# Optimization experiments

Hardware: AMD Instinct MI355X
Metric: run time of the kernel (lower is better)

## Reference

```python
import jax, jax.numpy as jnp
import numpy as np

B, T, D, H, C = 8, 1024, 1024, 16, 8  # batch, seq, d_model, heads, num_concepts
DK = D // H
LAMBD = 5.0


def setup_inputs() -> dict:
    key = jax.random.key(0)
    ks = jax.random.split(key, 14)
    s = 0.02
    return {
        "qa_concept": jax.random.normal(ks[0], (B, T, T, C), jnp.float32),
        "query": jax.random.normal(ks[1], (B, T, D), jnp.float32),
        "key": jax.random.normal(ks[2], (B, T, D), jnp.float32),
        "value": jax.random.normal(ks[3], (B, T, D), jnp.float32),
        "Wq": jax.random.normal(ks[4], (D, D), jnp.float32) * s,
        "bq": jnp.zeros((D,), jnp.float32),
        "Wk": jax.random.normal(ks[5], (D, D), jnp.float32) * s,
        "bk": jnp.zeros((D,), jnp.float32),
        "Wv": jax.random.normal(ks[6], (D, D), jnp.float32) * s,
        "bv": jnp.zeros((D,), jnp.float32),
        "Wo": jax.random.normal(ks[7], (D, D), jnp.float32) * s,
        "bo": jnp.zeros((D,), jnp.float32),
        "mask": jax.random.randint(ks[8], (B, T), 0, 2, jnp.int32),
    }


def reference(qa_concept, query, key, value, Wq, bq, Wk, bk, Wv, bv, Wo, bo, mask):
    # Linear projections (torch Linear: y = x @ W.T + b)
    q = (query @ Wq.T + bq).reshape(B, T, H, DK).transpose(0, 2, 1, 3)  # [B,H,T,dk]
    k = (key @ Wk.T + bk).reshape(B, T, H, DK).transpose(0, 2, 1, 3)
    v = (value @ Wv.T + bv).reshape(B, T, H, DK).transpose(0, 2, 1, 3)
    scores = jnp.einsum("bhqd,bhkd->bhqk", q, k) / jnp.sqrt(jnp.float32(DK))
    # concept bias added to first C heads only
    bias = LAMBD * jnp.transpose(qa_concept, (0, 3, 1, 2))  # [B,C,T,T]
    scores = scores.at[:, :C, :, :].add(bias)
    # mask: [B,T] -> [B,1,1,T], fill -1e9 where 0
    scores = jnp.where(mask[:, None, None, :] == 0, jnp.float32(-1e9), scores)
    attn = jax.nn.softmax(scores, axis=-1)  # dropout is identity in eval
    x = jnp.einsum("bhqk,bhkd->bhqd", attn, v)
    x = x.transpose(0, 2, 1, 3).reshape(B, T, D)
    return x @ Wo.T + bo
```

## Files before the change

kernel.cpp:

```cpp
#include <hip/hip_runtime.h>

#define B_  8
#define T_  1024
#define D_  1024
#define H_  16
#define DK_ 64
#define C_  8
#define N_  (B_*T_)

typedef __attribute__((ext_vector_type(8))) short bf16x8;
typedef __attribute__((ext_vector_type(4))) float f32x4;
typedef __attribute__((ext_vector_type(8))) unsigned short u16x8;
typedef __attribute__((ext_vector_type(4))) unsigned short u16x4;

__device__ __forceinline__ float bf2f(unsigned short u) {
  union { unsigned int i; float f; } x; x.i = ((unsigned int)u) << 16; return x.f;
}
__device__ __forceinline__ unsigned short f2bf(float f) {
  union { float f; unsigned int i; } x; x.f = f;
  unsigned int r = (x.i + 0x7fffu + ((x.i >> 16) & 1u)) >> 16;
  return (unsigned short)r;
}
__device__ __forceinline__ unsigned short f2h(float f) {
  union { _Float16 h; unsigned short u; } x; x.h = (_Float16)f; return x.u;
}
__device__ __forceinline__ float h2f(unsigned short u) {
  union { _Float16 h; unsigned short u; } x; x.u = u; return (float)x.h;
}

__device__ __forceinline__ void gl_lds16(const unsigned short* g, unsigned short* l) {
  __builtin_amdgcn_global_load_lds(
      (const __attribute__((address_space(1))) unsigned int*)g,
      (__attribute__((address_space(3))) unsigned int*)l,
      16, 0, 0);
}

__global__ __launch_bounds__(256) void cvt32to16(
    const float* __restrict__ in, unsigned short* __restrict__ out, int n4) {
  int tid = blockIdx.x * blockDim.x + threadIdx.x;
  int stride = gridDim.x * blockDim.x;
  const float4* in4 = (const float4*)in;
  u16x4* out4 = (u16x4*)out;
  for (int i = tid; i < n4; i += stride) {
    float4 v = in4[i];
    u16x4 o = { f2bf(v.x), f2bf(v.y), f2bf(v.z), f2bf(v.w) };
    out4[i] = o;
  }
}

__global__ __launch_bounds__(256) void transposeQa(
    const float* __restrict__ qa, unsigned short* __restrict__ qat) {
  int b = blockIdx.x >> 10, q = blockIdx.x & 1023;
  int t = threadIdx.x;
  __shared__ float L[8][132];
  const float* src = qa + ((size_t)(b*T_ + q))*T_*C_;
  for (int ch = 0; ch < 8; ++ch) {
    int k0 = ch*128;
    float4 v = *(const float4*)(src + (size_t)(k0 + (t>>1))*C_ + (t&1)*4);
    int c4 = (t&1)*4, kk = t>>1;
    L[c4+0][kk] = v.x; L[c4+1][kk] = v.y; L[c4+2][kk] = v.z; L[c4+3][kk] = v.w;
    __syncthreads();
    int c = t >> 5, kk2 = (t&31)*4;
    float4 p = *(const float4*)&L[c][kk2];
    u16x4 o = { f2h(p.x), f2h(p.y), f2h(p.z), f2h(p.w) };
    *(u16x4*)(qat + ((size_t)(b*C_ + c)*T_ + q)*T_ + k0 + kk2) = o;
    __syncthreads();
  }
}

__global__ __launch_bounds__(256) void transposeV(
    const unsigned short* __restrict__ V, unsigned short* __restrict__ Vt) {
  int bid = blockIdx.x;
  int tt = bid & 15;
  int bh = bid >> 4;
  int b = bh >> 4, h = bh & 15;
  __shared__ unsigned short L[64][72];
  int r  = threadIdx.x >> 3;
  int c8 = (threadIdx.x & 7) * 8;
  const unsigned short* src = V + ((size_t)(b*T_ + tt*64))*D_ + h*64;
#pragma unroll
  for (int p = 0; p < 2; ++p) {
    int rr = r + p*32;
    u16x8 v = *(const u16x8*)(src + (size_t)rr*D_ + c8);
    *(u16x8*)&L[rr][c8] = v;
  }
  __syncthreads();
  unsigned short* dst = Vt + ((size_t)bh*64)*T_ + tt*64;
#pragma unroll
  for (int p = 0; p < 2; ++p) {
    int d = r + p*32;
    u16x8 o;
#pragma unroll
    for (int i = 0; i < 8; ++i) o[i] = L[c8 + i][d];
    *(u16x8*)(dst + (size_t)d*T_ + c8) = o;
  }
}

template <bool OUT_F32>
__global__ __launch_bounds__(256) void gemm_lds(
    const unsigned short* __restrict__ X, const unsigned short* __restrict__ W,
    const float* __restrict__ bias, void* __restrict__ Yv) {
  __shared__ __align__(16) unsigned short As[128*32];
  __shared__ __align__(16) unsigned short Bs[128*32];
  int orig = (blockIdx.x & 7) * 64 + (blockIdx.x >> 3);
  int bm = orig >> 3, bn = orig & 7;
  int t = threadIdx.x, lane = t & 63, w = t >> 6;
  int wr = w >> 1, wc = w & 1;
  int r16 = lane & 15, kg = lane >> 4;

  int srow0 = lane >> 2;
  int scol  = (lane & 3) * 8;
  const unsigned short* Ab = X + (size_t)(bm*128)*D_ + scol;
  const unsigned short* Bb = W + (size_t)(bn*128)*D_ + scol;

  f32x4 acc[4][4];
#pragma unroll
  for (int m = 0; m < 4; ++m)
#pragma unroll
    for (int n = 0; n < 4; ++n) acc[m][n] = (f32x4){0.f,0.f,0.f,0.f};

  for (int k0 = 0; k0 < D_; k0 += 32) {
    __syncthreads();
#pragma unroll
    for (int c = 0; c < 2; ++c) {
      int cidx = w*2 + c;
      int row = cidx*16 + srow0;
      gl_lds16(Ab + (size_t)row*D_ + k0, As + cidx*512);
      gl_lds16(Bb + (size_t)row*D_ + k0, Bs + cidx*512);
    }
    __syncthreads();

    bf16x8 a[4], bb[4];
#pragma unroll
    for (int m = 0; m < 4; ++m)
      a[m] = *(const bf16x8*)(As + (wr*64 + m*16 + r16)*32 + kg*8);
#pragma unroll
    for (int n = 0; n < 4; ++n)
      bb[n] = *(const bf16x8*)(Bs + (wc*64 + n*16 + r16)*32 + kg*8);
#pragma unroll
    for (int m = 0; m < 4; ++m)
#pragma unroll
      for (int n = 0; n < 4; ++n)
        acc[m][n] = __builtin_amdgcn_mfma_f32_16x16x32_bf16(a[m], bb[n], acc[m][n], 0, 0, 0);
  }

#pragma unroll
  for (int n = 0; n < 4; ++n) {
    int col = bn*128 + wc*64 + n*16 + r16;
    float bv = bias[col];
#pragma unroll
    for (int m = 0; m < 4; ++m) {
      int row0 = bm*128 + wr*64 + m*16 + kg*4;
#pragma unroll
      for (int jj = 0; jj < 4; ++jj) {
        float rv = acc[m][n][jj] + bv;
        if constexpr (OUT_F32)
          ((float*)Yv)[(size_t)(row0 + jj)*D_ + col] = rv;
        else
          ((unsigned short*)Yv)[(size_t)(row0 + jj)*D_ + col] = f2bf(rv);
      }
    }
  }
}

__global__ __launch_bounds__(256, 3) void attn4(
    const unsigned short* __restrict__ Q, const unsigned short* __restrict__ K,
    const unsigned short* __restrict__ Vt, const unsigned short* __restrict__ qat,
    const int* __restrict__ mask, unsigned short* __restrict__ X) {
  int swzid = ((blockIdx.x & 7) << 7) | (blockIdx.x >> 3);
  int qt = swzid & 7, h = (swzid >> 3) & 15, b = swzid >> 7;
  int w = threadIdx.x >> 6, lane = threadIdx.x & 63;
  int r16 = lane & 15, kg = lane >> 4;
  int q0w = qt*128 + w*32;
  int bh = b*H_ + h;

  __shared__ unsigned short Ks[2][64][64];
  __shared__ unsigned short Vs[2][64][64];
  __shared__ unsigned int  P32[4][16][32];

  int rl = lane >> 3;
  int eo = ((lane & 7) * 8) ^ (rl << 3);
  const unsigned short* Kb = K + ((size_t)b*T_)*D_ + h*DK_;
  const unsigned short* Vb = Vt + ((size_t)bh*DK_)*T_;

  int sw16 = (r16 & 7) << 4;
  int ko0 = ((kg*16 +  0) ^ sw16) >> 1;
  int ko1 = ((kg*16 + 64) ^ sw16) >> 1;
  int sw32 = (r16 & 7) << 2;

  bf16x8 qfr[2][2];
#pragma unroll
  for (int qf = 0; qf < 2; ++qf) {
    const unsigned short* qrow = Q + ((size_t)b*T_ + q0w + qf*16 + r16)*D_ + h*DK_ + kg*8;
    qfr[qf][0] = *(const bf16x8*)qrow;
    qfr[qf][1] = *(const bf16x8*)(qrow + 32);
  }

  f32x4 acc[2][4];
#pragma unroll
  for (int qf = 0; qf < 2; ++qf)
#pragma unroll
    for (int db = 0; db < 4; ++db) acc[qf][db] = (f32x4){0.f,0.f,0.f,0.f};
  float mold[2] = {-3e38f, -3e38f};
  float lsum[2] = {0.f, 0.f};

  const int* mrow = mask + b*T_;
  const unsigned short* qab0 = qat + ((size_t)((b*C_ + h)*T_) + q0w + r16)*T_;

#pragma unroll
  for (int c = 0; c < 2; ++c) {
    int cc = w*2 + c;
    gl_lds16(Kb + (size_t)(cc*8 + rl)*D_ + eo, &Ks[0][cc*8][0]);
    gl_lds16(Vb + (size_t)(cc*8 + rl)*T_ + eo, &Vs[0][cc*8][0]);
  }
  __syncthreads();

  for (int t = 0; t < 16; ++t) {
    int k0 = t*64, bb = t & 1;
    if (t < 15) {
      int kn = k0 + 64, nb = bb ^ 1;
#pragma unroll
      for (int c = 0; c < 2; ++c) {
        int cc = w*2 + c;
        gl_lds16(Kb + (size_t)(kn + cc*8 + rl)*D_ + eo, &Ks[nb][cc*8][0]);
        gl_lds16(Vb + (size_t)(cc*8 + rl)*T_ + kn + eo, &Vs[nb][cc*8][0]);
      }
    }
    u16x4 qv[2][4];
    if (h < C_) {
#pragma unroll
      for (int qf = 0; qf < 2; ++qf)
#pragma unroll
        for (int kt = 0; kt < 4; ++kt)
          qv[qf][kt] = *(const u16x4*)(qab0 + (size_t)qf*16*T_ + k0 + kt*16 + kg*4);
    }
    int mk = mrow[k0 + lane];
    unsigned long long bits = __ballot(mk != 0);

    f32x4 s[2][4];
#pragma unroll
    for (int kt = 0; kt < 4; ++kt) {
      bf16x8 kf0 = *(const bf16x8*)&Ks[bb][kt*16 + r16][ko0];
      bf16x8 kf1 = *(const bf16x8*)&Ks[bb][kt*16 + r16][ko1];
#pragma unroll
      for (int qf = 0; qf < 2; ++qf) {
        f32x4 z = (f32x4){0.f,0.f,0.f,0.f};
        z = __builtin_amdgcn_mfma_f32_16x16x32_bf16(kf0, qfr[qf][0], z, 0, 0, 0);
        z = __builtin_amdgcn_mfma_f32_16x16x32_bf16(kf1, qfr[qf][1], z, 0, 0, 0);
        s[qf][kt] = z;
      }
    }

#pragma unroll
    for (int qf = 0; qf < 2; ++qf) {
      float pmax = -3e38f;
#pragma unroll
      for (int kt = 0; kt < 4; ++kt)
#pragma unroll
        for (int jj = 0; jj < 4; ++jj) {
          float v = s[qf][kt][jj] * 0.125f;
          if (h < C_) v += 5.0f * h2f(qv[qf][kt][jj]);
          int idx = kt*16 + kg*4 + jj;
          v = ((bits >> idx) & 1ULL) ? v : -1e9f;
          s[qf][kt][jj] = v;
          pmax = fmaxf(pmax, v);
        }
      pmax = fmaxf(pmax, __shfl_xor(pmax, 16, 64));
      pmax = fmaxf(pmax, __shfl_xor(pmax, 32, 64));
      float mnew = fmaxf(mold[qf], pmax);
      float sc = __expf(mold[qf] - mnew);
      mold[qf] = mnew;
      float psum = 0.f;
      unsigned int pk[8];
#pragma unroll
      for (int kt = 0; kt < 4; ++kt) {
        float p0 = __expf(s[qf][kt][0] - mnew), p1 = __expf(s[qf][kt][1] - mnew);
        float p2 = __expf(s[qf][kt][2] - mnew), p3 = __expf(s[qf][kt][3] - mnew);
        psum += (p0 + p1) + (p2 + p3);
        pk[kt*2+0] = (unsigned)f2bf(p0) | ((unsigned)f2bf(p1) << 16);
        pk[kt*2+1] = (unsigned)f2bf(p2) | ((unsigned)f2bf(p3) << 16);
      }
      psum += __shfl_xor(psum, 16, 64);
      psum += __shfl_xor(psum, 32, 64);
      lsum[qf] = lsum[qf] * sc + psum;
      float scq[4];
#pragma unroll
      for (int jj = 0; jj < 4; ++jj) scq[jj] = __shfl(sc, kg*4 + jj, 64);
#pragma unroll
      for (int db = 0; db < 4; ++db)
#pragma unroll
        for (int jj = 0; jj < 4; ++jj) acc[qf][db][jj] *= scq[jj];
#pragma unroll
      for (int kt = 0; kt < 4; ++kt)
        *(uint2*)&P32[w][r16][(kt*8 + kg*2) ^ sw32] =
            make_uint2(pk[kt*2], pk[kt*2+1]);
      __builtin_amdgcn_sched_barrier(0);
      asm volatile("s_waitcnt lgkmcnt(0)");
      __builtin_amdgcn_sched_barrier(0);
      bf16x8 pa0 = *(const bf16x8*)&P32[w][r16][(kg*4) ^ sw32];
      bf16x8 pa1 = *(const bf16x8*)&P32[w][r16][(16 + kg*4) ^ sw32];
#pragma unroll
      for (int db = 0; db < 4; ++db) {
        bf16x8 vf0 = *(const bf16x8*)&Vs[bb][db*16 + r16][ko0];
        bf16x8 vf1 = *(const bf16x8*)&Vs[bb][db*16 + r16][ko1];
        acc[qf][db] = __builtin_amdgcn_mfma_f32_16x16x32_bf16(pa0, vf0, acc[qf][db], 0, 0, 0);
        acc[qf][db] = __builtin_amdgcn_mfma_f32_16x16x32_bf16(pa1, vf1, acc[qf][db], 0, 0, 0);
      }
    }
    __syncthreads();
  }

#pragma unroll
  for (int qf = 0; qf < 2; ++qf) {
    float linv = 1.0f / lsum[qf];
    float invq[4];
#pragma unroll
    for (int jj = 0; jj < 4; ++jj) invq[jj] = __shfl(linv, kg*4 + jj, 64);
#pragma unroll
    for (int jj = 0; jj < 4; ++jj)
#pragma unroll
      for (int db = 0; db < 4; ++db)
        X[((size_t)b*T_ + q0w + qf*16 + kg*4 + jj)*D_ + h*DK_ + db*16 + r16] =
            f2bf(acc[qf][db][jj] * invq[jj]);
  }
}

__global__ __launch_bounds__(256) void attn_fused(
    const unsigned short* __restrict__ Q, const unsigned short* __restrict__ K,
    const unsigned short* __restrict__ Vt, const float* __restrict__ qa,
    const int* __restrict__ mask, unsigned short* __restrict__ X) {
  int bid = blockIdx.x;
  int qt = bid & 15, h = (bid >> 4) & 15, b = bid >> 8;
  int w = threadIdx.x >> 6, lane = threadIdx.x & 63;
  int r16 = lane & 15, kg = lane >> 4;
  int q0 = qt*64 + w*16;
  int bh = b*H_ + h;

  __shared__ unsigned short P[4][16][72];

  const unsigned short* qrow = Q + ((size_t)b*T_ + q0 + r16)*D_ + h*DK_ + kg*8;
  bf16x8 qf0 = *(const bf16x8*)qrow;
  bf16x8 qf1 = *(const bf16x8*)(qrow + 32);

  f32x4 acc[4];
#pragma unroll
  for (int db = 0; db < 4; ++db) acc[db] = (f32x4){0.f,0.f,0.f,0.f};
  float mrow[4], lrow[4];
#pragma unroll
  for (int jj = 0; jj < 4; ++jj) { mrow[jj] = -3e38f; lrow[jj] = 0.f; }

  const int* mptr = mask + b*T_;
  const unsigned short* Kbase = K + ((size_t)b*T_)*D_ + h*DK_;
  const unsigned short* Vbase = Vt + ((size_t)bh*DK_)*T_;
  const float* qabase = qa + ((size_t)(b*T_ + q0 + kg*4))*T_*C_ + h;

  for (int k0 = 0; k0 < T_; k0 += 64) {
    f32x4 s[4];
#pragma unroll
    for (int kt = 0; kt < 4; ++kt) {
      const unsigned short* krow = Kbase + (size_t)(k0 + kt*16 + r16)*D_ + kg*8;
      f32x4 z = (f32x4){0.f,0.f,0.f,0.f};
      z = __builtin_amdgcn_mfma_f32_16x16x32_bf16(qf0, *(const bf16x8*)krow,        z, 0, 0, 0);
      z = __builtin_amdgcn_mfma_f32_16x16x32_bf16(qf1, *(const bf16x8*)(krow + 32), z, 0, 0, 0);
      s[kt] = z;
    }
    int mk[4];
#pragma unroll
    for (int kt = 0; kt < 4; ++kt) mk[kt] = mptr[k0 + kt*16 + r16];
    if (h < C_) {
#pragma unroll
      for (int kt = 0; kt < 4; ++kt)
#pragma unroll
        for (int jj = 0; jj < 4; ++jj) {
          float bb = qabase[(size_t)jj*T_*C_ + (size_t)(k0 + kt*16 + r16)*C_];
          s[kt][jj] = s[kt][jj]*0.125f + 5.0f*bb;
        }
    } else {
#pragma unroll
      for (int kt = 0; kt < 4; ++kt)
#pragma unroll
        for (int jj = 0; jj < 4; ++jj) s[kt][jj] *= 0.125f;
    }
#pragma unroll
    for (int kt = 0; kt < 4; ++kt)
#pragma unroll
      for (int jj = 0; jj < 4; ++jj)
        if (mk[kt] == 0) s[kt][jj] = -1e9f;

#pragma unroll
    for (int jj = 0; jj < 4; ++jj) {
      float v = fmaxf(fmaxf(s[0][jj], s[1][jj]), fmaxf(s[2][jj], s[3][jj]));
#pragma unroll
      for (int d = 1; d < 16; d <<= 1) v = fmaxf(v, __shfl_xor(v, d, 64));
      float mnew = fmaxf(mrow[jj], v);
      float sc = __expf(mrow[jj] - mnew);
      mrow[jj] = mnew;
      lrow[jj] *= sc;
#pragma unroll
      for (int db = 0; db < 4; ++db) acc[db][jj] *= sc;
      float rs = 0.f;
#pragma unroll
      for (int kt = 0; kt < 4; ++kt) {
        float p = __expf(s[kt][jj] - mnew);
        rs += p;
        P[w][kg*4 + jj][kt*16 + r16] = f2bf(p);
      }
#pragma unroll
      for (int d = 1; d < 16; d <<= 1) rs += __shfl_xor(rs, d, 64);
      lrow[jj] += rs;
    }
    __syncthreads();

    bf16x8 pa0 = *(const bf16x8*)&P[w][r16][kg*8];
    bf16x8 pa1 = *(const bf16x8*)&P[w][r16][32 + kg*8];
#pragma unroll
    for (int db = 0; db < 4; ++db) {
      const unsigned short* vr = Vbase + (size_t)(db*16 + r16)*T_ + k0 + kg*8;
      acc[db] = __builtin_amdgcn_mfma_f32_16x16x32_bf16(pa0, *(const bf16x8*)vr,        acc[db], 0, 0, 0);
      acc[db] = __builtin_amdgcn_mfma_f32_16x16x32_bf16(pa1, *(const bf16x8*)(vr + 32), acc[db], 0, 0, 0);
    }
  }

  float inv[4];
#pragma unroll
  for (int jj = 0; jj < 4; ++jj) inv[jj] = 1.0f / lrow[jj];
#pragma unroll
  for (int jj = 0; jj < 4; ++jj)
#pragma unroll
    for (int db = 0; db < 4; ++db)
      X[((size_t)b*T_ + q0 + kg*4 + jj)*D_ + h*DK_ + db*16 + r16] =
          f2bf(acc[db][jj] * inv[jj]);
}

extern "C" void kernel_launch(void* const* d_in, const int* in_sizes, int n_in,
                              void* d_out, int out_size, void* d_ws, size_t ws_size,
                              hipStream_t stream) {
  const float* qa    = (const float*)d_in[0];
  const float* query = (const float*)d_in[1];
  const float* key   = (const float*)d_in[2];
  const float* value = (const float*)d_in[3];
  const float* Wq = (const float*)d_in[4];
  const float* bq = (const float*)d_in[5];
  const float* Wk = (const float*)d_in[6];
  const float* bk = (const float*)d_in[7];
  const float* Wv = (const float*)d_in[8];
  const float* bv = (const float*)d_in[9];
  const float* Wo = (const float*)d_in[10];
  const float* bo = (const float*)d_in[11];
  const int* mask = (const int*)d_in[12];

  const size_t ND = (size_t)N_ * D_;
  const size_t DD = (size_t)D_ * D_;
  const size_t QAT = (size_t)B_ * C_ * T_ * T_;
  unsigned short* Qws = (unsigned short*)d_ws;
  unsigned short* Kws = Qws + ND;
  unsigned short* Vws = Kws + ND;
  unsigned short* Xws = Vws + ND;
  unsigned short* qbf = Xws + ND;
  unsigned short* kbf = qbf + ND;
  unsigned short* vbf = kbf + ND;
  unsigned short* wqbf = vbf + ND;
  unsigned short* wkbf = wqbf + DD;
  unsigned short* wvbf = wkbf + DD;
  unsigned short* wobf = wvbf + DD;
  unsigned short* qatws = wobf + DD;
  unsigned short* Vtws = qbf;

  bool fast = ws_size >= (7*ND + 4*DD + QAT) * sizeof(unsigned short);

  dim3 blk(256);
  cvt32to16<<<2048, blk, 0, stream>>>(query, qbf, (int)(ND/4));
  cvt32to16<<<2048, blk, 0, stream>>>(key,   kbf, (int)(ND/4));
  cvt32to16<<<2048, blk, 0, stream>>>(value, vbf, (int)(ND/4));
  cvt32to16<<<512,  blk, 0, stream>>>(Wq, wqbf, (int)(DD/4));
  cvt32to16<<<512,  blk, 0, stream>>>(Wk, wkbf, (int)(DD/4));
  cvt32to16<<<512,  blk, 0, stream>>>(Wv, wvbf, (int)(DD/4));
  cvt32to16<<<512,  blk, 0, stream>>>(Wo, wobf, (int)(DD/4));

  int ggrid = (N_/128) * (D_/128);
  gemm_lds<false><<<ggrid, blk, 0, stream>>>(qbf, wqbf, bq, Qws);
  gemm_lds<false><<<ggrid, blk, 0, stream>>>(kbf, wkbf, bk, Kws);
  gemm_lds<false><<<ggrid, blk, 0, stream>>>(vbf, wvbf, bv, Vws);

  transposeV<<<B_*H_*(T_/64), blk, 0, stream>>>(Vws, Vtws);

  if (fast) {
    transposeQa<<<B_*T_, blk, 0, stream>>>(qa, qatws);
    attn4<<<B_*H_*(T_/128), blk, 0, stream>>>(Qws, Kws, Vtws, qatws, mask, Xws);
  } else {
    attn_fused<<<B_*H_*(T_/64), blk, 0, stream>>>(Qws, Kws, Vtws, qa, mask, Xws);
  }

  gemm_lds<true><<<ggrid, blk, 0, stream>>>(Xws, wobf, bo, (float*)d_out);
}
```

Measured before the change: 359.4 us.

## Add lazy softmax rescaling, interleave P staging with PV MFMAs, and set wave priority

The attention loop now rescales the running max and accumulator only when some row's new block max exceeds the old max by more than 8, and skips the rescale otherwise. It also restructures the two query fragments so V fragments load once and are shared, and the second P tile's LDS write overlaps the first fragment's PV MFMAs. s_setprio raises wave priority around the MFMA sections. The lazy rescale lets exponentials grow up to e^8 before a correction, which risks bf16/fp32 range issues only in extreme cases.

```diff
diff --git a/kernel.cpp b/kernel.cpp
--- a/kernel.cpp
+++ b/kernel.cpp
@@ -163,7 +163,7 @@
   }
 }
 
-__global__ __launch_bounds__(256, 3) void attn4(
+__global__ __launch_bounds__(256, 3) void attn5(
     const unsigned short* __restrict__ Q, const unsigned short* __restrict__ K,
     const unsigned short* __restrict__ Vt, const unsigned short* __restrict__ qat,
     const int* __restrict__ mask, unsigned short* __restrict__ X) {
@@ -238,6 +238,7 @@
     unsigned long long bits = __ballot(mk != 0);
 
     f32x4 s[2][4];
+    __builtin_amdgcn_s_setprio(1);
 #pragma unroll
     for (int kt = 0; kt < 4; ++kt) {
       bf16x8 kf0 = *(const bf16x8*)&Ks[bb][kt*16 + r16][ko0];
@@ -250,7 +251,9 @@
         s[qf][kt] = z;
       }
     }
-
+    __builtin_amdgcn_s_setprio(0);
+
+    float pmaxq[2];
 #pragma unroll
     for (int qf = 0; qf < 2; ++qf) {
       float pmax = -3e38f;
@@ -267,46 +270,87 @@
         }
       pmax = fmaxf(pmax, __shfl_xor(pmax, 16, 64));
       pmax = fmaxf(pmax, __shfl_xor(pmax, 32, 64));
-      float mnew = fmaxf(mold[qf], pmax);
-      float sc = __expf(mold[qf] - mnew);
-      mold[qf] = mnew;
-      float psum = 0.f;
-      unsigned int pk[8];
-#pragma unroll
-      for (int kt = 0; kt < 4; ++kt) {
-        float p0 = __expf(s[qf][kt][0] - mnew), p1 = __expf(s[qf][kt][1] - mnew);
-        float p2 = __expf(s[qf][kt][2] - mnew), p3 = __expf(s[qf][kt][3] - mnew);
-        psum += (p0 + p1) + (p2 + p3);
-        pk[kt*2+0] = (unsigned)f2bf(p0) | ((unsigned)f2bf(p1) << 16);
-        pk[kt*2+1] = (unsigned)f2bf(p2) | ((unsigned)f2bf(p3) << 16);
+      pmaxq[qf] = pmax;
+    }
+    if (!__all(pmaxq[0] - mold[0] <= 8.0f && pmaxq[1] - mold[1] <= 8.0f)) {
+#pragma unroll
+      for (int qf = 0; qf < 2; ++qf) {
+        float mnew = fmaxf(mold[qf], pmaxq[qf]);
+        float sc = __expf(mold[qf] - mnew);
+        mold[qf] = mnew;
+        lsum[qf] *= sc;
+        float scq[4];
+#pragma unroll
+        for (int jj = 0; jj < 4; ++jj) scq[jj] = __shfl(sc, kg*4 + jj, 64);
+#pragma unroll
+        for (int db = 0; db < 4; ++db)
+#pragma unroll
+          for (int jj = 0; jj < 4; ++jj) acc[qf][db][jj] *= scq[jj];
       }
-      psum += __shfl_xor(psum, 16, 64);
-      psum += __shfl_xor(psum, 32, 64);
-      lsum[qf] = lsum[qf] * sc + psum;
-      float scq[4];
-#pragma unroll
-      for (int jj = 0; jj < 4; ++jj) scq[jj] = __shfl(sc, kg*4 + jj, 64);
-#pragma unroll
-      for (int db = 0; db < 4; ++db)
-#pragma unroll
-        for (int jj = 0; jj < 4; ++jj) acc[qf][db][jj] *= scq[jj];
-#pragma unroll
-      for (int kt = 0; kt < 4; ++kt)
-        *(uint2*)&P32[w][r16][(kt*8 + kg*2) ^ sw32] =
-            make_uint2(pk[kt*2], pk[kt*2+1]);
-      __builtin_amdgcn_sched_barrier(0);
-      asm volatile("s_waitcnt lgkmcnt(0)");
-      __builtin_amdgcn_sched_barrier(0);
-      bf16x8 pa0 = *(const bf16x8*)&P32[w][r16][(kg*4) ^ sw32];
-      bf16x8 pa1 = *(const bf16x8*)&P32[w][r16][(16 + kg*4) ^ sw32];
-#pragma unroll
-      for (int db = 0; db < 4; ++db) {
-        bf16x8 vf0 = *(const bf16x8*)&Vs[bb][db*16 + r16][ko0];
-        bf16x8 vf1 = *(const bf16x8*)&Vs[bb][db*16 + r16][ko1];
-        acc[qf][db] = __builtin_amdgcn_mfma_f32_16x16x32_bf16(pa0, vf0, acc[qf][db], 0, 0, 0);
-        acc[qf][db] = __builtin_amdgcn_mfma_f32_16x16x32_bf16(pa1, vf1, acc[qf][db], 0, 0, 0);
-      }
-    }
+    }
+    unsigned int pk0[8], pk1[8];
+    float psum0 = 0.f;
+#pragma unroll
+    for (int kt = 0; kt < 4; ++kt) {
+      float p0 = __expf(s[0][kt][0] - mold[0]), p1 = __expf(s[0][kt][1] - mold[0]);
+      float p2 = __expf(s[0][kt][2] - mold[0]), p3 = __expf(s[0][kt][3] - mold[0]);
+      psum0 += (p0 + p1) + (p2 + p3);
+      pk0[kt*2+0] = (unsigned)f2bf(p0) | ((unsigned)f2bf(p1) << 16);
+      pk0[kt*2+1] = (unsigned)f2bf(p2) | ((unsigned)f2bf(p3) << 16);
+    }
+#pragma unroll
+    for (int kt = 0; kt < 4; ++kt)
+      *(uint2*)&P32[w][r16][(kt*8 + kg*2) ^ sw32] = make_uint2(pk0[kt*2], pk0[kt*2+1]);
+    float psum1 = 0.f;
+#pragma unroll
+    for (int kt = 0; kt < 4; ++kt) {
+      float p0 = __expf(s[1][kt][0] - mold[1]), p1 = __expf(s[1][kt][1] - mold[1]);
+      float p2 = __expf(s[1][kt][2] - mold[1]), p3 = __expf(s[1][kt][3] - mold[1]);
+      psum1 += (p0 + p1) + (p2 + p3);
+      pk1[kt*2+0] = (unsigned)f2bf(p0) | ((unsigned)f2bf(p1) << 16);
+      pk1[kt*2+1] = (unsigned)f2bf(p2) | ((unsigned)f2bf(p3) << 16);
+    }
+    psum0 += __shfl_xor(psum0, 16, 64);
+    psum0 += __shfl_xor(psum0, 32, 64);
+    psum1 += __shfl_xor(psum1, 16, 64);
+    psum1 += __shfl_xor(psum1, 32, 64);
+    lsum[0] += psum0;
+    lsum[1] += psum1;
+
+    __builtin_amdgcn_sched_barrier(0);
+    asm volatile("s_waitcnt lgkmcnt(0)");
+    __builtin_amdgcn_sched_barrier(0);
+    bf16x8 pa00 = *(const bf16x8*)&P32[w][r16][(kg*4) ^ sw32];
+    bf16x8 pa01 = *(const bf16x8*)&P32[w][r16][(16 + kg*4) ^ sw32];
+    bf16x8 vf[4][2];
+#pragma unroll
+    for (int db = 0; db < 4; ++db) {
+      vf[db][0] = *(const bf16x8*)&Vs[bb][db*16 + r16][ko0];
+      vf[db][1] = *(const bf16x8*)&Vs[bb][db*16 + r16][ko1];
+    }
+    __builtin_amdgcn_sched_barrier(0);
+#pragma unroll
+    for (int kt = 0; kt < 4; ++kt)
+      *(uint2*)&P32[w][r16][(kt*8 + kg*2) ^ sw32] = make_uint2(pk1[kt*2], pk1[kt*2+1]);
+    __builtin_amdgcn_s_setprio(1);
+#pragma unroll
+    for (int db = 0; db < 4; ++db) {
+      acc[0][db] = __builtin_amdgcn_mfma_f32_16x16x32_bf16(pa00, vf[db][0], acc[0][db], 0, 0, 0);
+      acc[0][db] = __builtin_amdgcn_mfma_f32_16x16x32_bf16(pa01, vf[db][1], acc[0][db], 0, 0, 0);
+    }
+    __builtin_amdgcn_s_setprio(0);
+    __builtin_amdgcn_sched_barrier(0);
+    asm volatile("s_waitcnt lgkmcnt(0)");
+    __builtin_amdgcn_sched_barrier(0);
+    bf16x8 pa10 = *(const bf16x8*)&P32[w][r16][(kg*4) ^ sw32];
+    bf16x8 pa11 = *(const bf16x8*)&P32[w][r16][(16 + kg*4) ^ sw32];
+    __builtin_amdgcn_s_setprio(1);
+#pragma unroll
+    for (int db = 0; db < 4; ++db) {
+      acc[1][db] = __builtin_amdgcn_mfma_f32_16x16x32_bf16(pa10, vf[db][0], acc[1][db], 0, 0, 0);
+      acc[1][db] = __builtin_amdgcn_mfma_f32_16x16x32_bf16(pa11, vf[db][1], acc[1][db], 0, 0, 0);
+    }
+    __builtin_amdgcn_s_setprio(0);
     __syncthreads();
   }
 
@@ -486,7 +530,7 @@
 
   if (fast) {
     transposeQa<<<B_*T_, blk, 0, stream>>>(qa, qatws);
-    attn4<<<B_*H_*(T_/128), blk, 0, stream>>>(Qws, Kws, Vtws, qatws, mask, Xws);
+    attn5<<<B_*H_*(T_/128), blk, 0, stream>>>(Qws, Kws, Vtws, qatws, mask, Xws);
   } else {
     attn_fused<<<B_*H_*(T_/64), blk, 0, stream>>>(Qws, Kws, Vtws, qa, mask, Xws);
   }
```

New measurement: 397.3 us. +10.6%, slower.

## Use lazy softmax rescaling and deferred row-sum reduction in attention kernel

Applied to the files above, without the earlier changes.

The online softmax now rescales the running max and accumulators only when some row's new tile max exceeds the stored max by more than 8, decided wave-wide with __all, so most tiles skip the exp and accumulator multiply. Row sums are kept as per-lane partials and reduced across lanes once at the end rather than every tile. The P buffer in LDS is doubled so both query fragments are written before a single lgkmcnt wait. In exchange, exponentials can reach up to e^8 before rescaling, which slightly raises bf16 rounding and overflow headroom concerns, and LDS use grows.

```diff
diff --git a/kernel.cpp b/kernel.cpp
--- a/kernel.cpp
+++ b/kernel.cpp
@@ -163,7 +163,7 @@
   }
 }
 
-__global__ __launch_bounds__(256, 3) void attn4(
+__global__ __launch_bounds__(256, 3) void attn4b(
     const unsigned short* __restrict__ Q, const unsigned short* __restrict__ K,
     const unsigned short* __restrict__ Vt, const unsigned short* __restrict__ qat,
     const int* __restrict__ mask, unsigned short* __restrict__ X) {
@@ -176,7 +176,7 @@
 
   __shared__ unsigned short Ks[2][64][64];
   __shared__ unsigned short Vs[2][64][64];
-  __shared__ unsigned int  P32[4][16][32];
+  __shared__ unsigned int  P32[4][2][16][32];
 
   int rl = lane >> 3;
   int eo = ((lane & 7) * 8) ^ (rl << 3);
@@ -202,7 +202,7 @@
 #pragma unroll
     for (int db = 0; db < 4; ++db) acc[qf][db] = (f32x4){0.f,0.f,0.f,0.f};
   float mold[2] = {-3e38f, -3e38f};
-  float lsum[2] = {0.f, 0.f};
+  float lpart[2] = {0.f, 0.f};
 
   const int* mrow = mask + b*T_;
   const unsigned short* qab0 = qat + ((size_t)((b*C_ + h)*T_) + q0w + r16)*T_;
@@ -251,6 +251,7 @@
       }
     }
 
+    float pmaxq[2];
 #pragma unroll
     for (int qf = 0; qf < 2; ++qf) {
       float pmax = -3e38f;
@@ -267,38 +268,47 @@
         }
       pmax = fmaxf(pmax, __shfl_xor(pmax, 16, 64));
       pmax = fmaxf(pmax, __shfl_xor(pmax, 32, 64));
-      float mnew = fmaxf(mold[qf], pmax);
-      float sc = __expf(mold[qf] - mnew);
-      mold[qf] = mnew;
-      float psum = 0.f;
+      pmaxq[qf] = pmax;
+    }
+    if (!__all(pmaxq[0] - mold[0] <= 8.0f && pmaxq[1] - mold[1] <= 8.0f)) {
+#pragma unroll
+      for (int qf = 0; qf < 2; ++qf) {
+        float mnew = fmaxf(mold[qf], pmaxq[qf]);
+        float sc = __expf(mold[qf] - mnew);
+        mold[qf] = mnew;
+        lpart[qf] *= sc;
+        float scq[4];
+#pragma unroll
+        for (int jj = 0; jj < 4; ++jj) scq[jj] = __shfl(sc, kg*4 + jj, 64);
+#pragma unroll
+        for (int db = 0; db < 4; ++db)
+#pragma unroll
+          for (int jj = 0; jj < 4; ++jj) acc[qf][db][jj] *= scq[jj];
+      }
+    }
+#pragma unroll
+    for (int qf = 0; qf < 2; ++qf) {
       unsigned int pk[8];
 #pragma unroll
       for (int kt = 0; kt < 4; ++kt) {
-        float p0 = __expf(s[qf][kt][0] - mnew), p1 = __expf(s[qf][kt][1] - mnew);
-        float p2 = __expf(s[qf][kt][2] - mnew), p3 = __expf(s[qf][kt][3] - mnew);
-        psum += (p0 + p1) + (p2 + p3);
+        float p0 = __expf(s[qf][kt][0] - mold[qf]), p1 = __expf(s[qf][kt][1] - mold[qf]);
+        float p2 = __expf(s[qf][kt][2] - mold[qf]), p3 = __expf(s[qf][kt][3] - mold[qf]);
+        lpart[qf] += (p0 + p1) + (p2 + p3);
         pk[kt*2+0] = (unsigned)f2bf(p0) | ((unsigned)f2bf(p1) << 16);
         pk[kt*2+1] = (unsigned)f2bf(p2) | ((unsigned)f2bf(p3) << 16);
       }
-      psum += __shfl_xor(psum, 16, 64);
-      psum += __shfl_xor(psum, 32, 64);
-      lsum[qf] = lsum[qf] * sc + psum;
-      float scq[4];
-#pragma unroll
-      for (int jj = 0; jj < 4; ++jj) scq[jj] = __shfl(sc, kg*4 + jj, 64);
-#pragma unroll
-      for (int db = 0; db < 4; ++db)
-#pragma unroll
-        for (int jj = 0; jj < 4; ++jj) acc[qf][db][jj] *= scq[jj];
 #pragma unroll
       for (int kt = 0; kt < 4; ++kt)
-        *(uint2*)&P32[w][r16][(kt*8 + kg*2) ^ sw32] =
+        *(uint2*)&P32[w][qf][r16][(kt*8 + kg*2) ^ sw32] =
             make_uint2(pk[kt*2], pk[kt*2+1]);
-      __builtin_amdgcn_sched_barrier(0);
-      asm volatile("s_waitcnt lgkmcnt(0)");
-      __builtin_amdgcn_sched_barrier(0);
-      bf16x8 pa0 = *(const bf16x8*)&P32[w][r16][(kg*4) ^ sw32];
-      bf16x8 pa1 = *(const bf16x8*)&P32[w][r16][(16 + kg*4) ^ sw32];
+    }
+    __builtin_amdgcn_sched_barrier(0);
+    asm volatile("s_waitcnt lgkmcnt(0)");
+    __builtin_amdgcn_sched_barrier(0);
+#pragma unroll
+    for (int qf = 0; qf < 2; ++qf) {
+      bf16x8 pa0 = *(const bf16x8*)&P32[w][qf][r16][(kg*4) ^ sw32];
+      bf16x8 pa1 = *(const bf16x8*)&P32[w][qf][r16][(16 + kg*4) ^ sw32];
 #pragma unroll
       for (int db = 0; db < 4; ++db) {
         bf16x8 vf0 = *(const bf16x8*)&Vs[bb][db*16 + r16][ko0];
@@ -312,7 +322,10 @@
 
 #pragma unroll
   for (int qf = 0; qf < 2; ++qf) {
-    float linv = 1.0f / lsum[qf];
+    float lp = lpart[qf];
+    lp += __shfl_xor(lp, 16, 64);
+    lp += __shfl_xor(lp, 32, 64);
+    float linv = 1.0f / lp;
     float invq[4];
 #pragma unroll
     for (int jj = 0; jj < 4; ++jj) invq[jj] = __shfl(linv, kg*4 + jj, 64);
@@ -486,7 +499,7 @@
 
   if (fast) {
     transposeQa<<<B_*T_, blk, 0, stream>>>(qa, qatws);
-    attn4<<<B_*H_*(T_/128), blk, 0, stream>>>(Qws, Kws, Vtws, qatws, mask, Xws);
+    attn4b<<<B_*H_*(T_/128), blk, 0, stream>>>(Qws, Kws, Vtws, qatws, mask, Xws);
   } else {
     attn_fused<<<B_*H_*(T_/64), blk, 0, stream>>>(Qws, Kws, Vtws, qa, mask, Xws);
   }
```

New measurement: 340.5 us. 1.06x faster.
